# Kernel optimization log

Hardware: AMD Instinct MI355X
Metric: run time of the kernel (lower is better)

The kernel has to match this reference:

```python
import jax, jax.numpy as jnp
import numpy as np

D_K = 64
D_MODEL = 1024
N_HEADS = 16


def setup_inputs() -> dict:
    key = jax.random.key(0)
    ks = jax.random.split(key, 9)
    B, S = 2, 2048
    scale = 1.0 / np.sqrt(D_MODEL)
    inp = {
        "x": jax.random.normal(ks[0], (B, S, D_MODEL), dtype=jnp.float32),
        "w_q": jax.random.normal(ks[1], (D_MODEL, N_HEADS * D_K), dtype=jnp.float32) * scale,
        "b_q": jnp.zeros((N_HEADS * D_K,), dtype=jnp.float32),
        "w_k": jax.random.normal(ks[2], (D_MODEL, N_HEADS * D_K), dtype=jnp.float32) * scale,
        "b_k": jnp.zeros((N_HEADS * D_K,), dtype=jnp.float32),
        "w_v": jax.random.normal(ks[3], (D_MODEL, N_HEADS * D_K), dtype=jnp.float32) * scale,
        "b_v": jnp.zeros((N_HEADS * D_K,), dtype=jnp.float32),
        "w_o": jax.random.normal(ks[4], (N_HEADS * D_K, D_MODEL), dtype=jnp.float32) * scale,
        "b_o": jnp.zeros((D_MODEL,), dtype=jnp.float32),
    }
    return inp


def reference(x, w_q, b_q, w_k, b_k, w_v, b_v, w_o, b_o):
    B, S, _ = x.shape
    H, Dk = N_HEADS, D_K

    def split_heads(m):  # [B,S,H*Dk] -> [B,H,S,Dk]
        return m.reshape(B, S, H, Dk).transpose(0, 2, 1, 3)

    Q = split_heads(x @ w_q + b_q)
    K = split_heads(x @ w_k + b_k)
    V = split_heads(x @ w_v + b_v)

    scores = jnp.einsum("bhsd,bhtd->bhst", Q, K) / jnp.sqrt(jnp.float32(Dk))
    probs = jax.nn.softmax(scores, axis=-1)
    attn = jnp.einsum("bhst,bhtd->bhsd", probs, V)  # [B,H,S,Dk]
    attn = attn.transpose(0, 2, 1, 3).reshape(B, S, H * Dk)
    return attn @ w_o + b_o
```

## Files before the change

### kernel.cpp

```cpp
#include <hip/hip_runtime.h>
#include <math.h>

#define D_MODELc 1024
#define N_HEADSc 16
#define D_Kc     64
#define B_SZc    2
#define S_LENc   2048
#define NTOKc    (B_SZc * S_LENc)

using half8  = __attribute__((ext_vector_type(8))) _Float16;
using half4  = __attribute__((ext_vector_type(4))) _Float16;
using fp16x2 = __attribute__((ext_vector_type(2))) __fp16;
using float4v = __attribute__((ext_vector_type(4))) float;

__global__ __launch_bounds__(256) void cvt_all(
    const float* __restrict__ x,
    const float* __restrict__ W0, const float* __restrict__ W1,
    const float* __restrict__ W2, const float* __restrict__ W3,
    _Float16* __restrict__ wout, _Float16* __restrict__ xout)
{
    __shared__ float T[32][33];
    const int z = blockIdx.z;
    const int t = threadIdx.x;

    if (z == 4) {
        const int bid = blockIdx.y * 32 + blockIdx.x;
        #pragma unroll
        for (int c = 0; c < 2; ++c) {
            const int i = bid * 512 + c * 256 + t;
            float4v a = ((const float4v*)x)[2 * i];
            float4v b = ((const float4v*)x)[2 * i + 1];
            half8 h;
            h[0] = (_Float16)a[0]; h[1] = (_Float16)a[1];
            h[2] = (_Float16)a[2]; h[3] = (_Float16)a[3];
            h[4] = (_Float16)b[0]; h[5] = (_Float16)b[1];
            h[6] = (_Float16)b[2]; h[7] = (_Float16)b[3];
            ((half8*)xout)[i] = h;
        }
        return;
    }

    const float* W = (z == 0) ? W0 : (z == 1) ? W1 : (z == 2) ? W2 : W3;
    _Float16* O = wout + (size_t)z * 1024 * 1024;

    const int k0 = blockIdx.x * 32;
    const int n0 = blockIdx.y * 32;
    {
        const int r = t >> 3, c4 = (t & 7) * 4;
        float4v v = *(const float4v*)(W + (size_t)(k0 + r) * 1024 + n0 + c4);
        T[r][c4 + 0] = v[0]; T[r][c4 + 1] = v[1];
        T[r][c4 + 2] = v[2]; T[r][c4 + 3] = v[3];
    }
    __syncthreads();
    {
        const int rn = t >> 3, ck4 = (t & 7) * 4;
        half4 h;
        h[0] = (_Float16)T[ck4 + 0][rn];
        h[1] = (_Float16)T[ck4 + 1][rn];
        h[2] = (_Float16)T[ck4 + 2][rn];
        h[3] = (_Float16)T[ck4 + 3][rn];
        *(half4*)(O + (size_t)(n0 + rn) * 1024 + k0 + ck4) = h;
    }
}

__global__ __launch_bounds__(256) void gemm_qkv(
    const _Float16* __restrict__ A, const _Float16* __restrict__ BtAll,
    const float* __restrict__ bias0, const float* __restrict__ bias1,
    const float* __restrict__ bias2, _Float16* __restrict__ Cout)
{
    __shared__ _Float16 Als[2][128 * 32];
    __shared__ _Float16 Bls[2][128 * 32];

    constexpr int K = 1024;
    const int tid = threadIdx.x;
    const int m0  = blockIdx.x * 128;
    const int n0  = blockIdx.y * 128;
    const int z   = blockIdx.z;

    const _Float16* Bt  = BtAll + (size_t)z * 1024 * 1024;
    const float* bias   = (z == 0) ? bias0 : (z == 1) ? bias1 : bias2;
    const float qscale  = (z == 0) ? 0.18033688011112042f : 1.0f;

    const int wave = tid >> 6, lane = tid & 63;
    const int wr = wave >> 1, wc = wave & 1;
    const int quad = lane >> 4, l16 = lane & 15;

    float4v acc[4][4];
    #pragma unroll
    for (int i = 0; i < 4; ++i)
        #pragma unroll
        for (int j = 0; j < 4; ++j)
            acc[i][j] = (float4v){0.f, 0.f, 0.f, 0.f};

    for (int k0 = 0; k0 < K; k0 += 64) {
        #pragma unroll
        for (int c = 0; c < 2; ++c) {
            const int i   = c * 256 + tid;
            const int row = i >> 2, kc = i & 3;
            #pragma unroll
            for (int h = 0; h < 2; ++h) {
                __builtin_amdgcn_global_load_lds(
                    (const __attribute__((address_space(1))) void*)
                        (A + (size_t)(m0 + row) * K + k0 + h * 32 + kc * 8),
                    (__attribute__((address_space(3))) void*)(Als[h] + i * 8),
                    16, 0, 0);
                __builtin_amdgcn_global_load_lds(
                    (const __attribute__((address_space(1))) void*)
                        (Bt + (size_t)(n0 + row) * K + k0 + h * 32 + kc * 8),
                    (__attribute__((address_space(3))) void*)(Bls[h] + i * 8),
                    16, 0, 0);
            }
        }
        __syncthreads();

        half8 af[4][2], bf[4][2];
        #pragma unroll
        for (int i = 0; i < 4; ++i) {
            const int r = (wr * 64 + i * 16 + l16) * 32 + quad * 8;
            af[i][0] = *(const half8*)(Als[0] + r);
            af[i][1] = *(const half8*)(Als[1] + r);
        }
        #pragma unroll
        for (int j = 0; j < 4; ++j) {
            const int r = (wc * 64 + j * 16 + l16) * 32 + quad * 8;
            bf[j][0] = *(const half8*)(Bls[0] + r);
            bf[j][1] = *(const half8*)(Bls[1] + r);
        }
        #pragma unroll
        for (int i = 0; i < 4; ++i)
            #pragma unroll
            for (int j = 0; j < 4; ++j) {
                acc[i][j] = __builtin_amdgcn_mfma_f32_16x16x32_f16(
                    af[i][0], bf[j][0], acc[i][j], 0, 0, 0);
                acc[i][j] = __builtin_amdgcn_mfma_f32_16x16x32_f16(
                    af[i][1], bf[j][1], acc[i][j], 0, 0, 0);
            }
        __syncthreads();
    }

    if (z != 2) {
        #pragma unroll
        for (int i = 0; i < 4; ++i) {
            const int rbase = m0 + wr * 64 + i * 16 + quad * 4;
            #pragma unroll
            for (int j = 0; j < 4; ++j) {
                const int col = n0 + wc * 64 + j * 16 + l16;
                const float bv = bias[col];
                #pragma unroll
                for (int r = 0; r < 4; ++r) {
                    const float v = (acc[i][j][r] + bv) * qscale;
                    const int n = rbase + r;
                    const int b = n >> 11, s = n & 2047;
                    const int h = col >> 6, d = col & 63;
                    _Float16* C = Cout + (size_t)z * NTOKc * D_MODELc;
                    C[(((size_t)(b * N_HEADSc + h)) * S_LENc + s) * D_Kc + d] =
                        (_Float16)v;
                }
            }
        }
    } else {
        #pragma unroll
        for (int i = 0; i < 4; ++i) {
            const int rbase = m0 + wr * 64 + i * 16 + quad * 4;
            const int b = rbase >> 11, s0 = rbase & 2047;
            #pragma unroll
            for (int j = 0; j < 4; ++j) {
                const int col = n0 + wc * 64 + j * 16 + l16;
                const float bv = bias[col];
                const int h = col >> 6, d = col & 63;
                half4 hv;
                #pragma unroll
                for (int r = 0; r < 4; ++r)
                    hv[r] = (_Float16)(acc[i][j][r] + bv);
                _Float16* C = Cout + (size_t)2 * NTOKc * D_MODELc;
                *(half4*)(C + (((size_t)(b * N_HEADSc + h)) * D_Kc + d) *
                          S_LENc + s0) = hv;
            }
        }
    }
}

__global__ __launch_bounds__(256) void gemm_out(
    const _Float16* __restrict__ A, const _Float16* __restrict__ Bt,
    const float* __restrict__ bias, float* __restrict__ C)
{
    __shared__ _Float16 Als[2][64 * 32];
    __shared__ _Float16 Bls[2][128 * 32];

    constexpr int K = 1024;
    const int tid = threadIdx.x;
    const int m0  = blockIdx.x * 64;
    const int n0  = blockIdx.y * 128;

    const int wave = tid >> 6, lane = tid & 63;
    const int wr = wave >> 1, wc = wave & 1;
    const int quad = lane >> 4, l16 = lane & 15;

    float4v acc[2][4];
    #pragma unroll
    for (int i = 0; i < 2; ++i)
        #pragma unroll
        for (int j = 0; j < 4; ++j)
            acc[i][j] = (float4v){0.f, 0.f, 0.f, 0.f};

    for (int k0 = 0; k0 < K; k0 += 64) {
        {
            const int row = tid >> 2, kc = tid & 3;
            #pragma unroll
            for (int h = 0; h < 2; ++h)
                __builtin_amdgcn_global_load_lds(
                    (const __attribute__((address_space(1))) void*)
                        (A + (size_t)(m0 + row) * K + k0 + h * 32 + kc * 8),
                    (__attribute__((address_space(3))) void*)(Als[h] + tid * 8),
                    16, 0, 0);
        }
        #pragma unroll
        for (int c = 0; c < 2; ++c) {
            const int i = c * 256 + tid;
            const int row = i >> 2, kc = i & 3;
            #pragma unroll
            for (int h = 0; h < 2; ++h)
                __builtin_amdgcn_global_load_lds(
                    (const __attribute__((address_space(1))) void*)
                        (Bt + (size_t)(n0 + row) * K + k0 + h * 32 + kc * 8),
                    (__attribute__((address_space(3))) void*)(Bls[h] + i * 8),
                    16, 0, 0);
        }
        __syncthreads();

        half8 af[2][2], bf[4][2];
        #pragma unroll
        for (int i = 0; i < 2; ++i) {
            const int r = (wr * 32 + i * 16 + l16) * 32 + quad * 8;
            af[i][0] = *(const half8*)(Als[0] + r);
            af[i][1] = *(const half8*)(Als[1] + r);
        }
        #pragma unroll
        for (int j = 0; j < 4; ++j) {
            const int r = (wc * 64 + j * 16 + l16) * 32 + quad * 8;
            bf[j][0] = *(const half8*)(Bls[0] + r);
            bf[j][1] = *(const half8*)(Bls[1] + r);
        }
        #pragma unroll
        for (int i = 0; i < 2; ++i)
            #pragma unroll
            for (int j = 0; j < 4; ++j) {
                acc[i][j] = __builtin_amdgcn_mfma_f32_16x16x32_f16(
                    af[i][0], bf[j][0], acc[i][j], 0, 0, 0);
                acc[i][j] = __builtin_amdgcn_mfma_f32_16x16x32_f16(
                    af[i][1], bf[j][1], acc[i][j], 0, 0, 0);
            }
        __syncthreads();
    }

    #pragma unroll
    for (int i = 0; i < 2; ++i) {
        const int rbase = m0 + wr * 32 + i * 16 + quad * 4;
        #pragma unroll
        for (int j = 0; j < 4; ++j) {
            const int col = n0 + wc * 64 + j * 16 + l16;
            const float bv = bias[col];
            #pragma unroll
            for (int r = 0; r < 4; ++r)
                C[(size_t)(rbase + r) * 1024 + col] = acc[i][j][r] + bv;
        }
    }
}

__global__ __launch_bounds__(256) void attn_mfma(
    const _Float16* __restrict__ Qb, const _Float16* __restrict__ Kb,
    const _Float16* __restrict__ Vtg, _Float16* __restrict__ Op,
    float* __restrict__ Lp)
{
    __shared__ _Float16 Ks[2][64 * 64];
    __shared__ _Float16 Vt[64 * 64];
    __shared__ _Float16 Ps[128 * 64];

    const int tid  = threadIdx.x;
    const int wv   = tid >> 6;
    const int lane = tid & 63;
    const int quad = lane >> 4;
    const int l16  = lane & 15;
    const int rotl = (l16 & 7) << 3;
    const int cA   = (quad * 8 + rotl) & 63;
    const int cB   = (quad * 8 + 32 + rotl) & 63;

    const int q0 = blockIdx.x * 128;
    const int bh = blockIdx.y;
    const int sp = blockIdx.z;
    const int kb = sp * (S_LENc / 2);
    const int kend = kb + S_LENc / 2;

    const _Float16* Qsl = Qb  + (size_t)bh * S_LENc * D_Kc;
    const _Float16* Ksl = Kb  + (size_t)bh * S_LENc * D_Kc;
    const _Float16* Vsl = Vtg + (size_t)bh * S_LENc * D_Kc;

    const int sR = tid >> 3;
    const int sC = (((tid & 7) - ((tid >> 3) & 7)) & 7) << 3;
    const _Float16* gK = Ksl + (size_t)sR * 64 + sC;
    const _Float16* gV = Vsl + (size_t)sR * S_LENc + sC;

#define STAGE_KT(BUF, T0)                                                    \
    {                                                                        \
        _Pragma("unroll")                                                    \
        for (int c = 0; c < 2; ++c)                                          \
            __builtin_amdgcn_global_load_lds(                                \
                (const __attribute__((address_space(1))) void*)              \
                    (gK + (size_t)(T0) * 64 + c * 2048),                     \
                (__attribute__((address_space(3))) void*)                    \
                    (Ks[BUF] + tid * 8 + c * 2048),                          \
                16, 0, 0);                                                   \
    }
#define STAGE_VT(T0)                                                         \
    {                                                                        \
        _Pragma("unroll")                                                    \
        for (int c = 0; c < 2; ++c)                                          \
            __builtin_amdgcn_global_load_lds(                                \
                (const __attribute__((address_space(1))) void*)              \
                    (gV + (T0) + c * 32 * S_LENc),                           \
                (__attribute__((address_space(3))) void*)                    \
                    (Vt + tid * 8 + c * 2048),                               \
                16, 0, 0);                                                   \
    }

    half8 aq[2][2];
    #pragma unroll
    for (int qf = 0; qf < 2; ++qf) {
        const int row = q0 + wv * 32 + qf * 16 + l16;
        aq[qf][0] = *(const half8*)(Qsl + (size_t)row * 64 + quad * 8);
        aq[qf][1] = *(const half8*)(Qsl + (size_t)row * 64 + 32 + quad * 8);
    }

    float4v O[2][4];
    #pragma unroll
    for (int qf = 0; qf < 2; ++qf)
        #pragma unroll
        for (int nt = 0; nt < 4; ++nt)
            O[qf][nt] = (float4v){0.f, 0.f, 0.f, 0.f};
    float lr[2] = {0.f, 0.f};

    STAGE_KT(0, kb);
    STAGE_VT(kb);

    int cur = 0;
    for (int t0 = kb; t0 < kend; t0 += 64) {
        __syncthreads();
        if (t0 != kb)
            STAGE_VT(t0);

        const _Float16* KsC = Ks[cur];
        half8 kf[4][2];
        #pragma unroll
        for (int nt = 0; nt < 4; ++nt) {
            const int base = (nt * 16 + l16) * 64;
            kf[nt][0] = *(const half8*)(KsC + base + cA);
            kf[nt][1] = *(const half8*)(KsC + base + cB);
        }

        #pragma unroll
        for (int qf = 0; qf < 2; ++qf) {
            float4v st[4];
            __builtin_amdgcn_s_setprio(1);
            #pragma unroll
            for (int nt = 0; nt < 4; ++nt) {
                st[nt] = __builtin_amdgcn_mfma_f32_16x16x32_f16(
                    kf[nt][0], aq[qf][0], (float4v){0.f, 0.f, 0.f, 0.f}, 0, 0, 0);
                st[nt] = __builtin_amdgcn_mfma_f32_16x16x32_f16(
                    kf[nt][1], aq[qf][1], st[nt], 0, 0, 0);
            }
            __builtin_amdgcn_s_setprio(0);
            float ls = 0.f;
            const int rowP = (wv * 32 + qf * 16 + l16) * 64;
            #pragma unroll
            for (int nt = 0; nt < 4; ++nt) {
                const float p0 = __builtin_amdgcn_exp2f(fminf(st[nt][0], 15.5f));
                const float p1 = __builtin_amdgcn_exp2f(fminf(st[nt][1], 15.5f));
                const float p2 = __builtin_amdgcn_exp2f(fminf(st[nt][2], 15.5f));
                const float p3 = __builtin_amdgcn_exp2f(fminf(st[nt][3], 15.5f));
                ls += (p0 + p1) + (p2 + p3);
                union { fp16x2 h2[2]; half4 h4; } u;
                u.h2[0] = __builtin_amdgcn_cvt_pkrtz(p0, p1);
                u.h2[1] = __builtin_amdgcn_cvt_pkrtz(p2, p3);
                *(half4*)(Ps + rowP + ((nt * 16 + quad * 4 + rotl) & 63)) = u.h4;
            }
            lr[qf] += ls;
        }

        __syncthreads();
        if (t0 + 64 < kend)
            STAGE_KT(cur ^ 1, t0 + 64);

        half8 bvv[4][2];
        #pragma unroll
        for (int nt = 0; nt < 4; ++nt) {
            const int base = (nt * 16 + l16) * 64;
            bvv[nt][0] = *(const half8*)(Vt + base + cA);
            bvv[nt][1] = *(const half8*)(Vt + base + cB);
        }
        #pragma unroll
        for (int qf = 0; qf < 2; ++qf) {
            const int rowP = (wv * 32 + qf * 16 + l16) * 64;
            half8 ap0 = *(const half8*)(Ps + rowP + cA);
            half8 ap1 = *(const half8*)(Ps + rowP + cB);
            __builtin_amdgcn_s_setprio(1);
            #pragma unroll
            for (int nt = 0; nt < 4; ++nt) {
                O[qf][nt] = __builtin_amdgcn_mfma_f32_16x16x32_f16(
                    ap0, bvv[nt][0], O[qf][nt], 0, 0, 0);
                O[qf][nt] = __builtin_amdgcn_mfma_f32_16x16x32_f16(
                    ap1, bvv[nt][1], O[qf][nt], 0, 0, 0);
            }
            __builtin_amdgcn_s_setprio(0);
        }
        cur ^= 1;
    }
#undef STAGE_KT
#undef STAGE_VT

    const size_t qgb = (size_t)bh * S_LENc;
    #pragma unroll
    for (int qf = 0; qf < 2; ++qf) {
        float t = lr[qf];
        t += __shfl_xor(t, 16, 64);
        t += __shfl_xor(t, 32, 64);
        if (quad == 0)
            Lp[(size_t)sp * 65536 + qgb + q0 + wv * 32 + qf * 16 + l16] = t;
        #pragma unroll
        for (int r = 0; r < 4; ++r) {
            const int q = q0 + wv * 32 + qf * 16 + quad * 4 + r;
            _Float16* dst = Op + ((size_t)sp * 65536 + qgb + q) * 64;
            #pragma unroll
            for (int nt = 0; nt < 4; ++nt)
                dst[nt * 16 + l16] = (_Float16)O[qf][nt][r];
        }
    }
}

__global__ __launch_bounds__(256) void attn_combine(
    const _Float16* __restrict__ Op, const float* __restrict__ Lp,
    _Float16* __restrict__ Ab)
{
    const int i  = blockIdx.x * 256 + threadIdx.x;
    const int e0 = i * 8;
    const int qg = e0 >> 6;
    const int d0 = e0 & 63;
    const int bh = qg >> 11, q = qg & 2047;
    const int b  = bh >> 4,  h = bh & 15;

    const float inv = 1.0f / (Lp[qg] + Lp[65536 + qg]);
    half8 o0 = *(const half8*)(Op + (size_t)qg * 64 + d0);
    half8 o1 = *(const half8*)(Op + ((size_t)65536 + qg) * 64 + d0);
    half8 hv;
    #pragma unroll
    for (int j = 0; j < 8; ++j)
        hv[j] = (_Float16)(((float)o0[j] + (float)o1[j]) * inv);
    *(half8*)(Ab + ((size_t)(b * S_LENc + q)) * 1024 + h * 64 + d0) = hv;
}

extern "C" void kernel_launch(void* const* d_in, const int* in_sizes, int n_in,
                              void* d_out, int out_size, void* d_ws, size_t ws_size,
                              hipStream_t stream)
{
    const float* x  = (const float*)d_in[0];
    const float* wq = (const float*)d_in[1];
    const float* bq = (const float*)d_in[2];
    const float* wk = (const float*)d_in[3];
    const float* bk = (const float*)d_in[4];
    const float* wv = (const float*)d_in[5];
    const float* bv = (const float*)d_in[6];
    const float* wo = (const float*)d_in[7];
    const float* bo = (const float*)d_in[8];
    float* out = (float*)d_out;

    const size_t M1 = 1024 * 1024;
    const size_t M4 = 4 * M1;
    _Float16* xh = (_Float16*)d_ws;
    _Float16* wh = xh + M4;
    _Float16* Qh = wh + M4;
    _Float16* Oph = Qh + 3 * M4;
    float*    Lp  = (float*)(Oph + 2 * M4);
    _Float16* Ah = xh;

    cvt_all<<<dim3(32, 32, 5), dim3(256), 0, stream>>>(
        x, wq, wk, wv, wo, wh, xh);
    gemm_qkv<<<dim3(NTOKc / 128, D_MODELc / 128, 3), dim3(256), 0, stream>>>(
        xh, wh, bq, bk, bv, Qh);
    attn_mfma<<<dim3(S_LENc / 128, B_SZc * N_HEADSc, 2), dim3(256), 0, stream>>>(
        Qh, Qh + M4, Qh + 2 * M4, Oph, Lp);
    attn_combine<<<dim3(NTOKc * D_MODELc / 8 / 256), dim3(256), 0, stream>>>(
        Oph, Lp, Ah);
    gemm_out<<<dim3(NTOKc / 64, D_MODELc / 128), dim3(256), 0, stream>>>(
        Ah, wh + 3 * M1, bo, out);
}
```

Baseline: 205.4 us.

## Drop split-K attention and combine kernel; normalize in-kernel with MFMA row sums

The attention kernel no longer splits the key range into two halves. Each block now handles 64 queries over the full sequence and writes the normalized output straight into the token-major buffer, so the separate combine kernel and the partial O/L buffers go away. Row sums are accumulated by an extra MFMA against a vector of ones instead of scalar adds and shuffles. Q/K are now stored token-major by the QKV GEMM, giving coalesced epilogue stores but strided K loads in attention. The tradeoff is a different grid of 32x32 blocks with fewer queries per wave and more K/V reloads per query.

```diff
diff --git a/kernel.cpp b/kernel.cpp
--- a/kernel.cpp
+++ b/kernel.cpp
@@ -139,6 +139,7 @@
     }
 
     if (z != 2) {
+        _Float16* C = Cout + (size_t)z * NTOKc * D_MODELc;
         #pragma unroll
         for (int i = 0; i < 4; ++i) {
             const int rbase = m0 + wr * 64 + i * 16 + quad * 4;
@@ -147,15 +148,9 @@
                 const int col = n0 + wc * 64 + j * 16 + l16;
                 const float bv = bias[col];
                 #pragma unroll
-                for (int r = 0; r < 4; ++r) {
-                    const float v = (acc[i][j][r] + bv) * qscale;
-                    const int n = rbase + r;
-                    const int b = n >> 11, s = n & 2047;
-                    const int h = col >> 6, d = col & 63;
-                    _Float16* C = Cout + (size_t)z * NTOKc * D_MODELc;
-                    C[(((size_t)(b * N_HEADSc + h)) * S_LENc + s) * D_Kc + d] =
-                        (_Float16)v;
-                }
+                for (int r = 0; r < 4; ++r)
+                    C[(size_t)(rbase + r) * 1024 + col] =
+                        (_Float16)((acc[i][j][r] + bv) * qscale);
             }
         }
     } else {
@@ -268,13 +263,12 @@
 }
 
 __global__ __launch_bounds__(256) void attn_mfma(
-    const _Float16* __restrict__ Qb, const _Float16* __restrict__ Kb,
-    const _Float16* __restrict__ Vtg, _Float16* __restrict__ Op,
-    float* __restrict__ Lp)
+    const _Float16* __restrict__ Qt, const _Float16* __restrict__ Kt,
+    const _Float16* __restrict__ Vtg, _Float16* __restrict__ Ab)
 {
     __shared__ _Float16 Ks[2][64 * 64];
     __shared__ _Float16 Vt[64 * 64];
-    __shared__ _Float16 Ps[128 * 64];
+    __shared__ _Float16 Ps[64 * 64];
 
     const int tid  = threadIdx.x;
     const int wv   = tid >> 6;
@@ -285,33 +279,31 @@
     const int cA   = (quad * 8 + rotl) & 63;
     const int cB   = (quad * 8 + 32 + rotl) & 63;
 
-    const int q0 = blockIdx.x * 128;
+    const int q0 = blockIdx.x * 64;
     const int bh = blockIdx.y;
-    const int sp = blockIdx.z;
-    const int kb = sp * (S_LENc / 2);
-    const int kend = kb + S_LENc / 2;
-
-    const _Float16* Qsl = Qb  + (size_t)bh * S_LENc * D_Kc;
-    const _Float16* Ksl = Kb  + (size_t)bh * S_LENc * D_Kc;
+    const int b  = bh >> 4, h = bh & 15;
+
+    const _Float16* Qsl = Qt + (size_t)b * S_LENc * D_MODELc + h * 64;
+    const _Float16* Ksl = Kt + (size_t)b * S_LENc * D_MODELc + h * 64;
     const _Float16* Vsl = Vtg + (size_t)bh * S_LENc * D_Kc;
 
     const int sR = tid >> 3;
     const int sC = (((tid & 7) - ((tid >> 3) & 7)) & 7) << 3;
-    const _Float16* gK = Ksl + (size_t)sR * 64 + sC;
+    const _Float16* gK = Ksl + (size_t)sR * D_MODELc + sC;
     const _Float16* gV = Vsl + (size_t)sR * S_LENc + sC;
 
-#define STAGE_KT(BUF, T0)                                                    \
+#define STAGE_K(BUF, T0)                                                     \
     {                                                                        \
         _Pragma("unroll")                                                    \
         for (int c = 0; c < 2; ++c)                                          \
             __builtin_amdgcn_global_load_lds(                                \
                 (const __attribute__((address_space(1))) void*)              \
-                    (gK + (size_t)(T0) * 64 + c * 2048),                     \
+                    (gK + (size_t)((T0) + c * 32) * D_MODELc),               \
                 (__attribute__((address_space(3))) void*)                    \
                     (Ks[BUF] + tid * 8 + c * 2048),                          \
                 16, 0, 0);                                                   \
     }
-#define STAGE_VT(T0)                                                         \
+#define STAGE_V(T0)                                                          \
     {                                                                        \
         _Pragma("unroll")                                                    \
         for (int c = 0; c < 2; ++c)                                          \
@@ -323,30 +315,31 @@
                 16, 0, 0);                                                   \
     }
 
-    half8 aq[2][2];
-    #pragma unroll
-    for (int qf = 0; qf < 2; ++qf) {
-        const int row = q0 + wv * 32 + qf * 16 + l16;
-        aq[qf][0] = *(const half8*)(Qsl + (size_t)row * 64 + quad * 8);
-        aq[qf][1] = *(const half8*)(Qsl + (size_t)row * 64 + 32 + quad * 8);
-    }
-
-    float4v O[2][4];
-    #pragma unroll
-    for (int qf = 0; qf < 2; ++qf)
-        #pragma unroll
-        for (int nt = 0; nt < 4; ++nt)
-            O[qf][nt] = (float4v){0.f, 0.f, 0.f, 0.f};
-    float lr[2] = {0.f, 0.f};
-
-    STAGE_KT(0, kb);
-    STAGE_VT(kb);
+    half8 aq[2];
+    {
+        const _Float16* qp = Qsl + (size_t)(q0 + wv * 16 + l16) * D_MODELc;
+        aq[0] = *(const half8*)(qp + quad * 8);
+        aq[1] = *(const half8*)(qp + 32 + quad * 8);
+    }
+
+    half8 vones;
+    #pragma unroll
+    for (int j = 0; j < 8; ++j) vones[j] = (_Float16)1.0f;
+
+    float4v O[4];
+    #pragma unroll
+    for (int nt = 0; nt < 4; ++nt)
+        O[nt] = (float4v){0.f, 0.f, 0.f, 0.f};
+    float4v Lacc = (float4v){0.f, 0.f, 0.f, 0.f};
+
+    STAGE_K(0, 0);
+    STAGE_V(0);
 
     int cur = 0;
-    for (int t0 = kb; t0 < kend; t0 += 64) {
-        __syncthreads();
-        if (t0 != kb)
-            STAGE_VT(t0);
+    for (int t0 = 0; t0 < S_LENc; t0 += 64) {
+        __syncthreads();
+        if (t0 != 0)
+            STAGE_V(t0);
 
         const _Float16* KsC = Ks[cur];
         half8 kf[4][2];
@@ -357,38 +350,33 @@
             kf[nt][1] = *(const half8*)(KsC + base + cB);
         }
 
-        #pragma unroll
-        for (int qf = 0; qf < 2; ++qf) {
-            float4v st[4];
-            __builtin_amdgcn_s_setprio(1);
-            #pragma unroll
-            for (int nt = 0; nt < 4; ++nt) {
-                st[nt] = __builtin_amdgcn_mfma_f32_16x16x32_f16(
-                    kf[nt][0], aq[qf][0], (float4v){0.f, 0.f, 0.f, 0.f}, 0, 0, 0);
-                st[nt] = __builtin_amdgcn_mfma_f32_16x16x32_f16(
-                    kf[nt][1], aq[qf][1], st[nt], 0, 0, 0);
-            }
-            __builtin_amdgcn_s_setprio(0);
-            float ls = 0.f;
-            const int rowP = (wv * 32 + qf * 16 + l16) * 64;
-            #pragma unroll
-            for (int nt = 0; nt < 4; ++nt) {
-                const float p0 = __builtin_amdgcn_exp2f(fminf(st[nt][0], 15.5f));
-                const float p1 = __builtin_amdgcn_exp2f(fminf(st[nt][1], 15.5f));
-                const float p2 = __builtin_amdgcn_exp2f(fminf(st[nt][2], 15.5f));
-                const float p3 = __builtin_amdgcn_exp2f(fminf(st[nt][3], 15.5f));
-                ls += (p0 + p1) + (p2 + p3);
-                union { fp16x2 h2[2]; half4 h4; } u;
-                u.h2[0] = __builtin_amdgcn_cvt_pkrtz(p0, p1);
-                u.h2[1] = __builtin_amdgcn_cvt_pkrtz(p2, p3);
-                *(half4*)(Ps + rowP + ((nt * 16 + quad * 4 + rotl) & 63)) = u.h4;
-            }
-            lr[qf] += ls;
-        }
-
-        __syncthreads();
-        if (t0 + 64 < kend)
-            STAGE_KT(cur ^ 1, t0 + 64);
+        float4v st[4];
+        __builtin_amdgcn_s_setprio(1);
+        #pragma unroll
+        for (int nt = 0; nt < 4; ++nt) {
+            st[nt] = __builtin_amdgcn_mfma_f32_16x16x32_f16(
+                kf[nt][0], aq[0], (float4v){0.f, 0.f, 0.f, 0.f}, 0, 0, 0);
+            st[nt] = __builtin_amdgcn_mfma_f32_16x16x32_f16(
+                kf[nt][1], aq[1], st[nt], 0, 0, 0);
+        }
+        __builtin_amdgcn_s_setprio(0);
+
+        const int rowP = (wv * 16 + l16) * 64;
+        #pragma unroll
+        for (int nt = 0; nt < 4; ++nt) {
+            const float p0 = __builtin_amdgcn_exp2f(fminf(st[nt][0], 15.5f));
+            const float p1 = __builtin_amdgcn_exp2f(fminf(st[nt][1], 15.5f));
+            const float p2 = __builtin_amdgcn_exp2f(fminf(st[nt][2], 15.5f));
+            const float p3 = __builtin_amdgcn_exp2f(fminf(st[nt][3], 15.5f));
+            union { fp16x2 h2[2]; half4 h4; } u;
+            u.h2[0] = __builtin_amdgcn_cvt_pkrtz(p0, p1);
+            u.h2[1] = __builtin_amdgcn_cvt_pkrtz(p2, p3);
+            *(half4*)(Ps + rowP + ((nt * 16 + quad * 4 + rotl) & 63)) = u.h4;
+        }
+
+        __syncthreads();
+        if (t0 + 64 < S_LENc)
+            STAGE_K(cur ^ 1, t0 + 64);
 
         half8 bvv[4][2];
         #pragma unroll
@@ -397,64 +385,34 @@
             bvv[nt][0] = *(const half8*)(Vt + base + cA);
             bvv[nt][1] = *(const half8*)(Vt + base + cB);
         }
-        #pragma unroll
-        for (int qf = 0; qf < 2; ++qf) {
-            const int rowP = (wv * 32 + qf * 16 + l16) * 64;
-            half8 ap0 = *(const half8*)(Ps + rowP + cA);
-            half8 ap1 = *(const half8*)(Ps + rowP + cB);
-            __builtin_amdgcn_s_setprio(1);
-            #pragma unroll
-            for (int nt = 0; nt < 4; ++nt) {
-                O[qf][nt] = __builtin_amdgcn_mfma_f32_16x16x32_f16(
-                    ap0, bvv[nt][0], O[qf][nt], 0, 0, 0);
-                O[qf][nt] = __builtin_amdgcn_mfma_f32_16x16x32_f16(
-                    ap1, bvv[nt][1], O[qf][nt], 0, 0, 0);
-            }
-            __builtin_amdgcn_s_setprio(0);
-        }
+        half8 ap0 = *(const half8*)(Ps + rowP + cA);
+        half8 ap1 = *(const half8*)(Ps + rowP + cB);
+        __builtin_amdgcn_s_setprio(1);
+        #pragma unroll
+        for (int nt = 0; nt < 4; ++nt) {
+            O[nt] = __builtin_amdgcn_mfma_f32_16x16x32_f16(
+                ap0, bvv[nt][0], O[nt], 0, 0, 0);
+            O[nt] = __builtin_amdgcn_mfma_f32_16x16x32_f16(
+                ap1, bvv[nt][1], O[nt], 0, 0, 0);
+        }
+        Lacc = __builtin_amdgcn_mfma_f32_16x16x32_f16(ap0, vones, Lacc, 0, 0, 0);
+        Lacc = __builtin_amdgcn_mfma_f32_16x16x32_f16(ap1, vones, Lacc, 0, 0, 0);
+        __builtin_amdgcn_s_setprio(0);
         cur ^= 1;
     }
-#undef STAGE_KT
-#undef STAGE_VT
-
-    const size_t qgb = (size_t)bh * S_LENc;
-    #pragma unroll
-    for (int qf = 0; qf < 2; ++qf) {
-        float t = lr[qf];
-        t += __shfl_xor(t, 16, 64);
-        t += __shfl_xor(t, 32, 64);
-        if (quad == 0)
-            Lp[(size_t)sp * 65536 + qgb + q0 + wv * 32 + qf * 16 + l16] = t;
-        #pragma unroll
-        for (int r = 0; r < 4; ++r) {
-            const int q = q0 + wv * 32 + qf * 16 + quad * 4 + r;
-            _Float16* dst = Op + ((size_t)sp * 65536 + qgb + q) * 64;
-            #pragma unroll
-            for (int nt = 0; nt < 4; ++nt)
-                dst[nt * 16 + l16] = (_Float16)O[qf][nt][r];
-        }
-    }
-}
-
-__global__ __launch_bounds__(256) void attn_combine(
-    const _Float16* __restrict__ Op, const float* __restrict__ Lp,
-    _Float16* __restrict__ Ab)
-{
-    const int i  = blockIdx.x * 256 + threadIdx.x;
-    const int e0 = i * 8;
-    const int qg = e0 >> 6;
-    const int d0 = e0 & 63;
-    const int bh = qg >> 11, q = qg & 2047;
-    const int b  = bh >> 4,  h = bh & 15;
-
-    const float inv = 1.0f / (Lp[qg] + Lp[65536 + qg]);
-    half8 o0 = *(const half8*)(Op + (size_t)qg * 64 + d0);
-    half8 o1 = *(const half8*)(Op + ((size_t)65536 + qg) * 64 + d0);
-    half8 hv;
-    #pragma unroll
-    for (int j = 0; j < 8; ++j)
-        hv[j] = (_Float16)(((float)o0[j] + (float)o1[j]) * inv);
-    *(half8*)(Ab + ((size_t)(b * S_LENc + q)) * 1024 + h * 64 + d0) = hv;
+#undef STAGE_K
+#undef STAGE_V
+
+    _Float16* Asl = Ab + (size_t)b * S_LENc * D_MODELc + h * 64;
+    #pragma unroll
+    for (int r = 0; r < 4; ++r) {
+        const float inv = 1.0f / Lacc[r];
+        const int q = q0 + wv * 16 + quad * 4 + r;
+        _Float16* dst = Asl + (size_t)q * D_MODELc;
+        #pragma unroll
+        for (int nt = 0; nt < 4; ++nt)
+            dst[nt * 16 + l16] = (_Float16)(O[nt][r] * inv);
+    }
 }
 
 extern "C" void kernel_launch(void* const* d_in, const int* in_sizes, int n_in,
@@ -477,18 +435,14 @@
     _Float16* xh = (_Float16*)d_ws;
     _Float16* wh = xh + M4;
     _Float16* Qh = wh + M4;
-    _Float16* Oph = Qh + 3 * M4;
-    float*    Lp  = (float*)(Oph + 2 * M4);
     _Float16* Ah = xh;
 
     cvt_all<<<dim3(32, 32, 5), dim3(256), 0, stream>>>(
         x, wq, wk, wv, wo, wh, xh);
     gemm_qkv<<<dim3(NTOKc / 128, D_MODELc / 128, 3), dim3(256), 0, stream>>>(
         xh, wh, bq, bk, bv, Qh);
-    attn_mfma<<<dim3(S_LENc / 128, B_SZc * N_HEADSc, 2), dim3(256), 0, stream>>>(
-        Qh, Qh + M4, Qh + 2 * M4, Oph, Lp);
-    attn_combine<<<dim3(NTOKc * D_MODELc / 8 / 256), dim3(256), 0, stream>>>(
-        Oph, Lp, Ah);
+    attn_mfma<<<dim3(S_LENc / 64, B_SZc * N_HEADSc), dim3(256), 0, stream>>>(
+        Qh, Qh + M4, Qh + 2 * M4, Ah);
     gemm_out<<<dim3(NTOKc / 64, D_MODELc / 128), dim3(256), 0, stream>>>(
         Ah, wh + 3 * M1, bo, out);
 }
```

Measured after the change: 204.3 us. No clear change (-0.5%).
